# Kernel tuning notes

Measured on AMD Instinct MI355X. Metric: run time of the kernel, lower is better.

The kernel has to match this reference:

```python
import jax, jax.numpy as jnp
import numpy as np

SCALE = 2.0 / 0.24  # UniformBoxWarp(sidelength=0.24)

def pos_embed(x, max_logscale, n_freqs):
    freqs = 2.0 ** jnp.linspace(0.0, float(max_logscale), n_freqs).astype(x.dtype)
    xb = x[..., None, :] * freqs[:, None]                  # (b, n, F, 3)
    sc = jnp.stack([jnp.sin(xb), jnp.cos(xb)], axis=-2)    # (b, n, F, 2, 3)
    sc = sc.reshape(x.shape[:-1] + (n_freqs * 2 * 3,))
    return jnp.concatenate([x, sc], axis=-1)

def film(x, W, b, freq, phase):
    # x: (b, n, in); freq/phase: (b, out) broadcast over points
    h = jnp.einsum('bni,oi->bno', x, W) + b
    return jnp.sin(freq[:, None, :] * h + phase[:, None, :])

def split_style(style):
    # rearrange 'b (2 d) -> b d 2'; freq = first half * 15 + 30, phase = second half
    d = style.shape[-1] // 2
    return style[:, :d] * 15.0 + 30.0, style[:, d:]

def setup_inputs() -> dict:
    key = jax.random.key(0)
    ks = jax.random.split(key, 14)
    B, N, H = 4, 65536, 256
    dim_pos, dim_dir = 63, 27
    r = lambda k, shp, s=1.0: jax.random.normal(k, shp, dtype=jnp.float32) * s
    return {
        'input': r(ks[0], (B, N, 3)),
        'ray_directions': r(ks[1], (B, N, 3)),
        'style_network': r(ks[2], (B, 4 * H)),
        'style_color': r(ks[3], (B, 2 * H)),
        'W1': r(ks[4], (H, dim_pos), 1.0 / dim_pos),
        'b1': jnp.zeros((H,), jnp.float32),
        'W2': r(ks[5], (H, H), np.sqrt(6.0 / H) / 25.0),
        'b2': jnp.zeros((H,), jnp.float32),
        'Wf': r(ks[6], (1, H), np.sqrt(6.0 / H) / 25.0),
        'bf': jnp.zeros((1,), jnp.float32),
        'Wcs': r(ks[7], (H, H + dim_dir), np.sqrt(6.0 / (H + dim_dir)) / 25.0),
        'bcs': jnp.zeros((H,), jnp.float32),
        'Wcl': r(ks[8], (3, H), np.sqrt(6.0 / H) / 25.0),
        'bcl': jnp.zeros((3,), jnp.float32),
    }

def reference(input, ray_directions, style_network, style_color,
              W1, b1, W2, b2, Wf, bf, Wcs, bcs, Wcl, bcl):
    H = W1.shape[0]
    pe = pos_embed(input * SCALE, 9, 10)                 # (b, n, 63)
    fn, pn = split_style(style_network)                  # (b, 2H) each
    x = film(pe, W1, b1, fn[:, :H], pn[:, :H])
    x = film(x, W2, b2, fn[:, H:], pn[:, H:])
    sigma = jnp.einsum('bnh,oh->bno', x, Wf) + bf        # (b, n, 1)
    de = pos_embed(ray_directions, 3, 4)                 # (b, n, 27)
    fc, pc = split_style(style_color)
    hc = film(jnp.concatenate([de, x], axis=-1), Wcs, bcs, fc, pc)
    rgb = jnp.einsum('bnh,oh->bno', hc, Wcl) + bcl       # (b, n, 3)
    return jnp.concatenate([rgb, sigma], axis=-1)        # (b, n, 4)
```

## Files before the change

### kernel.cpp

```cpp
#include <hip/hip_runtime.h>


#define SCALE_F 8.333333333333334f

typedef __attribute__((ext_vector_type(8)))  short sh8;
typedef __attribute__((ext_vector_type(16))) float f32x16;

__device__ __forceinline__ float redrev(float x) {
  const float chi = 0.15915494309189535f;
  const float clo = 6.4206383e-09f;
  float n = rintf(x * chi);
  float d = __builtin_fmaf(x, chi, -n);
  return __builtin_fmaf(x, clo, d);
}
__device__ __forceinline__ float fsin(float x) { return __builtin_amdgcn_sinf(redrev(x)); }
__device__ __forceinline__ float fcos(float x) { return __builtin_amdgcn_cosf(redrev(x)); }

__device__ __forceinline__ unsigned short bfh(float v) {
  unsigned u = __float_as_uint(v);
  return (unsigned short)((u + 0x7fffu + ((u >> 16) & 1u)) >> 16);
}
__device__ __forceinline__ float bf2f(unsigned short h) {
  return __uint_as_float(((unsigned)h) << 16);
}

__global__ void prep_w(const float* __restrict__ W1, const float* __restrict__ W2,
                       const float* __restrict__ Wcs, unsigned short* __restrict__ wsu)
{
  int t = blockIdx.x * 256 + threadIdx.x;
  if (t >= 155648) return;
  int L, pos, base;
  if (t < 16384)      { L = 0; pos = t;         base = 0; }
  else if (t < 81920) { L = 1; pos = t - 16384; base = 32768; }
  else                { L = 2; pos = t - 81920; base = 163840; }
  int kstep = pos >> 12, r = pos & 4095;
  int ot = (r >> 9) & 7, kh = (r >> 8) & 1, o5 = (r >> 3) & 31, j = r & 7;
  int o = ot * 32 + o5, k = kstep * 16 + kh * 8 + j;
  float wv = 0.f;
  if (L == 0)      { if (k < 63) wv = W1[o * 63 + k]; }
  else if (L == 1) { wv = W2[o * 256 + k]; }
  else             { if (k < 27) wv = Wcs[o * 283 + k];
                     else if (k >= 32) wv = Wcs[o * 283 + k - 5]; }
  unsigned short h = bfh(wv);
  unsigned short lo = bfh(wv - bf2f(h));
  wsu[base + kstep * 8192 + r] = h;
  wsu[base + kstep * 8192 + 4096 + r] = lo;
}

template <int NREG>
__device__ __forceinline__ void mfma_layer(
    const unsigned short* __restrict__ prep, int nk,
    const uint4* rBh, const uint4* rBl,
    unsigned short* lW, const unsigned short* lX,
    int myp, int lh, int l31, int ow, int tid, f32x16* acc)
{
  {
    const float4* s = (const float4*)prep;
    ((float4*)lW)[tid] = s[tid];
    ((float4*)lW)[tid + 512] = s[tid + 512];
  }
  __syncthreads();
  #pragma unroll 1
  for (int ks = 0; ks < nk; ++ks) {
    float4 pf0, pf1;
    const bool pre = (ks + 1) < nk;
    if (pre) {
      const float4* s = (const float4*)(prep + (size_t)(ks + 1) * 8192);
      pf0 = s[tid]; pf1 = s[tid + 512];
    }
    sh8 Bh, Bl;
    if (NREG > 0 && ks < NREG) {
      uint4 h = {0,0,0,0}, l = {0,0,0,0};
      #pragma unroll
      for (int rr = 0; rr < NREG; ++rr) if (ks == rr) { h = rBh[rr]; l = rBl[rr]; }
      Bh = __builtin_bit_cast(sh8, h); Bl = __builtin_bit_cast(sh8, l);
    } else {
      const int c0 = (((ks - NREG) * 16 + lh * 8) ^ ((myp & 15) << 3));
      Bh = *(const sh8*)&lX[myp * 256 + c0];
      Bl = *(const sh8*)&lX[32768 + myp * 256 + c0];
    }
    #pragma unroll
    for (int o = 0; o < 4; ++o) {
      const int wb = (ow * 4 + o) * 512 + lh * 256 + l31 * 8;
      sh8 Ah = *(const sh8*)&lW[wb];
      sh8 Al = *(const sh8*)&lW[4096 + wb];
      acc[o] = __builtin_amdgcn_mfma_f32_32x32x16_bf16(Ah, Bh, acc[o], 0, 0, 0);
      acc[o] = __builtin_amdgcn_mfma_f32_32x32x16_bf16(Al, Bh, acc[o], 0, 0, 0);
      acc[o] = __builtin_amdgcn_mfma_f32_32x32x16_bf16(Ah, Bl, acc[o], 0, 0, 0);
    }
    __syncthreads();
    if (pre) { ((float4*)lW)[tid] = pf0; ((float4*)lW)[tid + 512] = pf1; }
    __syncthreads();
  }
}

__device__ __forceinline__ float4 film_g(float4 fr, float4 ph, float a0, float a1, float a2, float a3) {
  float4 r;
  r.x = fsin(__builtin_fmaf(__builtin_fmaf(fr.x, 15.f, 30.f), a0, ph.x));
  r.y = fsin(__builtin_fmaf(__builtin_fmaf(fr.y, 15.f, 30.f), a1, ph.y));
  r.z = fsin(__builtin_fmaf(__builtin_fmaf(fr.z, 15.f, 30.f), a2, ph.z));
  r.w = fsin(__builtin_fmaf(__builtin_fmaf(fr.w, 15.f, 30.f), a3, ph.w));
  return r;
}
__device__ __forceinline__ void store_g(unsigned short* lX, int idx, float4 v) {
  unsigned short h0 = bfh(v.x), h1 = bfh(v.y), h2 = bfh(v.z), h3 = bfh(v.w);
  *(uint2*)&lX[idx] = make_uint2((unsigned)h0 | ((unsigned)h1 << 16),
                                 (unsigned)h2 | ((unsigned)h3 << 16));
  unsigned short l0 = bfh(v.x - bf2f(h0)), l1 = bfh(v.y - bf2f(h1));
  unsigned short l2 = bfh(v.z - bf2f(h2)), l3 = bfh(v.w - bf2f(h3));
  *(uint2*)&lX[32768 + idx] = make_uint2((unsigned)l0 | ((unsigned)l1 << 16),
                                         (unsigned)l2 | ((unsigned)l3 << 16));
}

__global__ void __launch_bounds__(512, 2)
siren_mfma(const float* __restrict__ input, const float* __restrict__ rdir,
           const float* __restrict__ sn, const float* __restrict__ sc,
           const float* __restrict__ b1, const float* __restrict__ b2,
           const float* __restrict__ Wf, const float* __restrict__ bfp,
           const float* __restrict__ bcs, const float* __restrict__ Wcl,
           const float* __restrict__ bcl, const unsigned short* __restrict__ wsu,
           float* __restrict__ out)
{
  __shared__ __align__(16) unsigned short lW[8192];
  __shared__ __align__(16) unsigned short lX[65536];
  __shared__ float lP[8][32][4];

  const int tid = threadIdx.x;
  const int w = tid >> 6, l = tid & 63;
  const int pw = w >> 1, ow = w & 1;
  const int l31 = l & 31, lh = l >> 5;
  const int gpt0 = blockIdx.x * 128;
  const int b = gpt0 >> 16;
  const int myp = pw * 32 + l31;
  const int gp = gpt0 + myp;
  const float* snb = sn + b * 1024;
  const float* scb = sc + b * 512;
  const int swz = (myp & 15) << 3;

  uint4 peh[4], pel[4], deh[2], del[2];
  {
    const float* ip = input + (size_t)gp * 3;
    float x0 = ip[0] * SCALE_F, x1 = ip[1] * SCALE_F, x2 = ip[2] * SCALE_F;
    const float* rp = rdir + (size_t)gp * 3;
    float r0 = rp[0], r1 = rp[1], r2 = rp[2];
    #pragma unroll
    for (int ks = 0; ks < 4; ++ks) {
      unsigned short hh[8], ll[8];
      #pragma unroll
      for (int j = 0; j < 8; ++j) {
        int k = ks * 16 + lh * 8 + j;
        float val;
        if (k >= 63) val = 0.f;
        else if (k < 3) val = (k == 0) ? x0 : (k == 1 ? x1 : x2);
        else {
          int rr = k - 3, f = rr / 6, rem = rr - f * 6;
          int d = (rem < 3) ? rem : rem - 3;
          float xa = (d == 0) ? x0 : (d == 1 ? x1 : x2);
          float arg = xa * (float)(1 << f);
          val = (rem < 3) ? fsin(arg) : fcos(arg);
        }
        hh[j] = bfh(val); ll[j] = bfh(val - bf2f(hh[j]));
      }
      peh[ks] = make_uint4((unsigned)hh[0] | ((unsigned)hh[1] << 16), (unsigned)hh[2] | ((unsigned)hh[3] << 16),
                           (unsigned)hh[4] | ((unsigned)hh[5] << 16), (unsigned)hh[6] | ((unsigned)hh[7] << 16));
      pel[ks] = make_uint4((unsigned)ll[0] | ((unsigned)ll[1] << 16), (unsigned)ll[2] | ((unsigned)ll[3] << 16),
                           (unsigned)ll[4] | ((unsigned)ll[5] << 16), (unsigned)ll[6] | ((unsigned)ll[7] << 16));
    }
    #pragma unroll
    for (int ks = 0; ks < 2; ++ks) {
      unsigned short hh[8], ll[8];
      #pragma unroll
      for (int j = 0; j < 8; ++j) {
        int k = ks * 16 + lh * 8 + j;
        float val;
        if (k >= 27) val = 0.f;
        else if (k < 3) val = (k == 0) ? r0 : (k == 1 ? r1 : r2);
        else {
          int rr = k - 3, f = rr / 6, rem = rr - f * 6;
          int d = (rem < 3) ? rem : rem - 3;
          float ra = (d == 0) ? r0 : (d == 1 ? r1 : r2);
          float arg = ra * (float)(1 << f);
          val = (rem < 3) ? fsin(arg) : fcos(arg);
        }
        hh[j] = bfh(val); ll[j] = bfh(val - bf2f(hh[j]));
      }
      deh[ks] = make_uint4((unsigned)hh[0] | ((unsigned)hh[1] << 16), (unsigned)hh[2] | ((unsigned)hh[3] << 16),
                           (unsigned)hh[4] | ((unsigned)hh[5] << 16), (unsigned)hh[6] | ((unsigned)hh[7] << 16));
      del[ks] = make_uint4((unsigned)ll[0] | ((unsigned)ll[1] << 16), (unsigned)ll[2] | ((unsigned)ll[3] << 16),
                           (unsigned)ll[4] | ((unsigned)ll[5] << 16), (unsigned)ll[6] | ((unsigned)ll[7] << 16));
    }
  }

  f32x16 acc[4];

  #pragma unroll
  for (int o = 0; o < 4; ++o) {
    #pragma unroll
    for (int g = 0; g < 4; ++g) {
      int ob = (ow * 4 + o) * 32 + g * 8 + lh * 4;
      float4 bv = *(const float4*)&b1[ob];
      acc[o][g * 4 + 0] = bv.x; acc[o][g * 4 + 1] = bv.y;
      acc[o][g * 4 + 2] = bv.z; acc[o][g * 4 + 3] = bv.w;
    }
  }
  mfma_layer<4>(wsu + 0, 4, peh, pel, lW, lX, myp, lh, l31, ow, tid, acc);
  #pragma unroll
  for (int o = 0; o < 4; ++o) {
    #pragma unroll
    for (int g = 0; g < 4; ++g) {
      int ob = (ow * 4 + o) * 32 + g * 8 + lh * 4;
      float4 fr = *(const float4*)&snb[ob];
      float4 ph = *(const float4*)&snb[512 + ob];
      float4 vv = film_g(fr, ph, acc[o][g*4+0], acc[o][g*4+1], acc[o][g*4+2], acc[o][g*4+3]);
      store_g(lX, myp * 256 + (ob ^ swz), vv);
    }
  }

  #pragma unroll
  for (int o = 0; o < 4; ++o) {
    #pragma unroll
    for (int g = 0; g < 4; ++g) {
      int ob = (ow * 4 + o) * 32 + g * 8 + lh * 4;
      float4 bv = *(const float4*)&b2[ob];
      acc[o][g * 4 + 0] = bv.x; acc[o][g * 4 + 1] = bv.y;
      acc[o][g * 4 + 2] = bv.z; acc[o][g * 4 + 3] = bv.w;
    }
  }
  mfma_layer<0>(wsu + 32768, 16, nullptr, nullptr, lW, lX, myp, lh, l31, ow, tid, acc);
  float sp = 0.f;
  #pragma unroll
  for (int o = 0; o < 4; ++o) {
    #pragma unroll
    for (int g = 0; g < 4; ++g) {
      int ob = (ow * 4 + o) * 32 + g * 8 + lh * 4;
      float4 fr = *(const float4*)&snb[256 + ob];
      float4 ph = *(const float4*)&snb[768 + ob];
      float4 vv = film_g(fr, ph, acc[o][g*4+0], acc[o][g*4+1], acc[o][g*4+2], acc[o][g*4+3]);
      float4 wf = *(const float4*)&Wf[ob];
      sp = __builtin_fmaf(wf.x, vv.x, sp); sp = __builtin_fmaf(wf.y, vv.y, sp);
      sp = __builtin_fmaf(wf.z, vv.z, sp); sp = __builtin_fmaf(wf.w, vv.w, sp);
      store_g(lX, myp * 256 + (ob ^ swz), vv);
    }
  }
  sp += __shfl_xor(sp, 32);
  lP[w][l31][3] = sp;

  #pragma unroll
  for (int o = 0; o < 4; ++o) {
    #pragma unroll
    for (int g = 0; g < 4; ++g) {
      int ob = (ow * 4 + o) * 32 + g * 8 + lh * 4;
      float4 bv = *(const float4*)&bcs[ob];
      acc[o][g * 4 + 0] = bv.x; acc[o][g * 4 + 1] = bv.y;
      acc[o][g * 4 + 2] = bv.z; acc[o][g * 4 + 3] = bv.w;
    }
  }
  mfma_layer<2>(wsu + 163840, 18, deh, del, lW, lX, myp, lh, l31, ow, tid, acc);
  float q0 = 0.f, q1 = 0.f, q2 = 0.f;
  #pragma unroll
  for (int o = 0; o < 4; ++o) {
    #pragma unroll
    for (int g = 0; g < 4; ++g) {
      int ob = (ow * 4 + o) * 32 + g * 8 + lh * 4;
      float4 fr = *(const float4*)&scb[ob];
      float4 ph = *(const float4*)&scb[256 + ob];
      float4 vv = film_g(fr, ph, acc[o][g*4+0], acc[o][g*4+1], acc[o][g*4+2], acc[o][g*4+3]);
      float4 w0 = *(const float4*)&Wcl[ob];
      float4 w1 = *(const float4*)&Wcl[256 + ob];
      float4 w2 = *(const float4*)&Wcl[512 + ob];
      q0 = __builtin_fmaf(w0.x, vv.x, q0); q0 = __builtin_fmaf(w0.y, vv.y, q0);
      q0 = __builtin_fmaf(w0.z, vv.z, q0); q0 = __builtin_fmaf(w0.w, vv.w, q0);
      q1 = __builtin_fmaf(w1.x, vv.x, q1); q1 = __builtin_fmaf(w1.y, vv.y, q1);
      q1 = __builtin_fmaf(w1.z, vv.z, q1); q1 = __builtin_fmaf(w1.w, vv.w, q1);
      q2 = __builtin_fmaf(w2.x, vv.x, q2); q2 = __builtin_fmaf(w2.y, vv.y, q2);
      q2 = __builtin_fmaf(w2.z, vv.z, q2); q2 = __builtin_fmaf(w2.w, vv.w, q2);
    }
  }
  q0 += __shfl_xor(q0, 32); q1 += __shfl_xor(q1, 32); q2 += __shfl_xor(q2, 32);
  lP[w][l31][0] = q0; lP[w][l31][1] = q1; lP[w][l31][2] = q2;
  __syncthreads();

  {
    int pt = tid >> 2, ch = tid & 3, pv = pt >> 5;
    float v = lP[pv * 2][pt & 31][ch] + lP[pv * 2 + 1][pt & 31][ch];
    v += (ch == 3) ? bfp[0] : bcl[ch];
    out[(size_t)gpt0 * 4 + tid] = v;
  }
}

extern "C" void kernel_launch(void* const* d_in, const int* in_sizes, int n_in,
                              void* d_out, int out_size, void* d_ws, size_t ws_size,
                              hipStream_t stream) {
  const float* input = (const float*)d_in[0];
  const float* rdir  = (const float*)d_in[1];
  const float* sn    = (const float*)d_in[2];
  const float* sc    = (const float*)d_in[3];
  const float* W1    = (const float*)d_in[4];
  const float* b1    = (const float*)d_in[5];
  const float* W2    = (const float*)d_in[6];
  const float* b2    = (const float*)d_in[7];
  const float* Wf    = (const float*)d_in[8];
  const float* bf    = (const float*)d_in[9];
  const float* Wcs   = (const float*)d_in[10];
  const float* bcs   = (const float*)d_in[11];
  const float* Wcl   = (const float*)d_in[12];
  const float* bcl   = (const float*)d_in[13];
  unsigned short* wsu = (unsigned short*)d_ws;
  float* out = (float*)d_out;

  prep_w<<<608, 256, 0, stream>>>(W1, W2, Wcs, wsu);
  siren_mfma<<<2048, 512, 0, stream>>>(input, rdir, sn, sc, b1, b2, Wf, bf,
                                       bcs, Wcl, bcl, wsu, out);
}
```

Measured before the change: 333.7 us.

## Switch split-precision MFMA to fp16 with scaled residuals and 2x2 wave tiling

Replaces the bf16 hi/lo split with an fp16 hi plus a 1024-scaled fp16 residual for both weights and activations. Each wave now computes 2 output tiles × 2 point tiles instead of 4 output tiles × 1 point tile, which changes per-wave data reuse. The positional embedding is now staged cooperatively through LDS, and the sine argument reduction is folded into the FiLM constants. Shared memory grows to about 144KB, dropping occupancy to one block per CU. The fp16 residual scaling also risks reduced range or underflow precision.

```diff
diff --git a/kernel.cpp b/kernel.cpp
--- a/kernel.cpp
+++ b/kernel.cpp
@@ -3,7 +3,8 @@
 
 #define SCALE_F 8.333333333333334f
 
-typedef __attribute__((ext_vector_type(8)))  short sh8;
+typedef _Float16 hf;
+typedef __attribute__((ext_vector_type(8)))  _Float16 hf8;
 typedef __attribute__((ext_vector_type(16))) float f32x16;
 
 __device__ __forceinline__ float redrev(float x) {
@@ -15,13 +16,18 @@
 }
 __device__ __forceinline__ float fsin(float x) { return __builtin_amdgcn_sinf(redrev(x)); }
 __device__ __forceinline__ float fcos(float x) { return __builtin_amdgcn_cosf(redrev(x)); }
-
-__device__ __forceinline__ unsigned short bfh(float v) {
-  unsigned u = __float_as_uint(v);
-  return (unsigned short)((u + 0x7fffu + ((u >> 16) & 1u)) >> 16);
-}
-__device__ __forceinline__ float bf2f(unsigned short h) {
-  return __uint_as_float(((unsigned)h) << 16);
+__device__ __forceinline__ float sinrev(float t) { return __builtin_amdgcn_sinf(t - rintf(t)); }
+
+#define INV2PI 0.15915494309189535f
+#define C15R   2.3873241463784303f
+#define C30R   4.7746482927568605f
+
+__device__ __forceinline__ unsigned pk2h(hf a, hf b) {
+  return ((unsigned)__builtin_bit_cast(unsigned short, a)) |
+         (((unsigned)__builtin_bit_cast(unsigned short, b)) << 16);
+}
+__device__ __forceinline__ int swadr(int pt, int slot) {
+  return pt * 256 + ((slot ^ (pt & 7)) << 3);
 }
 
 __global__ void prep_w(const float* __restrict__ W1, const float* __restrict__ W2,
@@ -39,54 +45,79 @@
   float wv = 0.f;
   if (L == 0)      { if (k < 63) wv = W1[o * 63 + k]; }
   else if (L == 1) { wv = W2[o * 256 + k]; }
-  else             { if (k < 27) wv = Wcs[o * 283 + k];
-                     else if (k >= 32) wv = Wcs[o * 283 + k - 5]; }
-  unsigned short h = bfh(wv);
-  unsigned short lo = bfh(wv - bf2f(h));
-  wsu[base + kstep * 8192 + r] = h;
-  wsu[base + kstep * 8192 + 4096 + r] = lo;
-}
-
-template <int NREG>
-__device__ __forceinline__ void mfma_layer(
-    const unsigned short* __restrict__ prep, int nk,
-    const uint4* rBh, const uint4* rBl,
-    unsigned short* lW, const unsigned short* lX,
-    int myp, int lh, int l31, int ow, int tid, f32x16* acc)
+  else { if (k < 256) wv = Wcs[o * 283 + 27 + k];
+         else { int q = k - 256; if (q < 27) wv = Wcs[o * 283 + q]; } }
+  hf hh = (hf)wv;
+  hf ll = (hf)((wv - (float)hh) * 1024.0f);
+  wsu[base + kstep * 8192 + r]        = __builtin_bit_cast(unsigned short, hh);
+  wsu[base + kstep * 8192 + 4096 + r] = __builtin_bit_cast(unsigned short, ll);
+}
+
+__device__ __forceinline__ float peval(float x0, float x1, float x2, int k) {
+  if (k >= 63) return 0.f;
+  if (k < 3) return (k == 0) ? x0 : ((k == 1) ? x1 : x2);
+  int rr = k - 3, f = rr / 6, rem = rr - f * 6;
+  int d = (rem < 3) ? rem : rem - 3;
+  float xa = (d == 0) ? x0 : ((d == 1) ? x1 : x2);
+  float arg = xa * (float)(1 << f);
+  return (rem < 3) ? fsin(arg) : fcos(arg);
+}
+__device__ __forceinline__ float deval(float r0, float r1, float r2, int k) {
+  if (k >= 27) return 0.f;
+  if (k < 3) return (k == 0) ? r0 : ((k == 1) ? r1 : r2);
+  int rr = k - 3, f = rr / 6, rem = rr - f * 6;
+  int d = (rem < 3) ? rem : rem - 3;
+  float ra = (d == 0) ? r0 : ((d == 1) ? r1 : r2);
+  float arg = ra * (float)(1 << f);
+  return (rem < 3) ? fsin(arg) : fcos(arg);
+}
+
+template <int NK, bool DE>
+__device__ __forceinline__ void layer_loop(
+    const unsigned short* __restrict__ prep,
+    unsigned short* __restrict__ lW, const unsigned short* __restrict__ lX,
+    f32x16 acc[2][2], int tid, int ow, int ptA, int ptB, int h, int l31,
+    const hf8* deBh, const hf8* deBl)
 {
   {
-    const float4* s = (const float4*)prep;
-    ((float4*)lW)[tid] = s[tid];
-    ((float4*)lW)[tid + 512] = s[tid + 512];
+    const float4* s0 = (const float4*)prep;
+    ((float4*)lW)[tid] = s0[tid];
+    ((float4*)lW)[tid + 512] = s0[tid + 512];
   }
   __syncthreads();
   #pragma unroll 1
-  for (int ks = 0; ks < nk; ++ks) {
+  for (int ks = 0; ks < NK; ++ks) {
     float4 pf0, pf1;
-    const bool pre = (ks + 1) < nk;
+    const bool pre = (ks + 1) < NK;
     if (pre) {
       const float4* s = (const float4*)(prep + (size_t)(ks + 1) * 8192);
       pf0 = s[tid]; pf1 = s[tid + 512];
     }
-    sh8 Bh, Bl;
-    if (NREG > 0 && ks < NREG) {
-      uint4 h = {0,0,0,0}, l = {0,0,0,0};
-      #pragma unroll
-      for (int rr = 0; rr < NREG; ++rr) if (ks == rr) { h = rBh[rr]; l = rBl[rr]; }
-      Bh = __builtin_bit_cast(sh8, h); Bl = __builtin_bit_cast(sh8, l);
+    hf8 Bh0, Bh1, Bl0, Bl1;
+    if (!DE || ks < NK - 2) {
+      Bh0 = *(const hf8*)&lX[swadr(ptA, ks * 2 + h)];
+      Bh1 = *(const hf8*)&lX[swadr(ptB, ks * 2 + h)];
+      Bl0 = *(const hf8*)&lX[32768 + swadr(ptA, ks * 2 + h)];
+      Bl1 = *(const hf8*)&lX[32768 + swadr(ptB, ks * 2 + h)];
     } else {
-      const int c0 = (((ks - NREG) * 16 + lh * 8) ^ ((myp & 15) << 3));
-      Bh = *(const sh8*)&lX[myp * 256 + c0];
-      Bl = *(const sh8*)&lX[32768 + myp * 256 + c0];
-    }
-    #pragma unroll
-    for (int o = 0; o < 4; ++o) {
-      const int wb = (ow * 4 + o) * 512 + lh * 256 + l31 * 8;
-      sh8 Ah = *(const sh8*)&lW[wb];
-      sh8 Al = *(const sh8*)&lW[4096 + wb];
-      acc[o] = __builtin_amdgcn_mfma_f32_32x32x16_bf16(Ah, Bh, acc[o], 0, 0, 0);
-      acc[o] = __builtin_amdgcn_mfma_f32_32x32x16_bf16(Al, Bh, acc[o], 0, 0, 0);
-      acc[o] = __builtin_amdgcn_mfma_f32_32x32x16_bf16(Ah, Bl, acc[o], 0, 0, 0);
+      int ksl = ks - (NK - 2);
+      Bh0 = deBh[ksl * 2 + 0]; Bh1 = deBh[ksl * 2 + 1];
+      Bl0 = deBl[ksl * 2 + 0]; Bl1 = deBl[ksl * 2 + 1];
+    }
+    const hf sc = (hf)0.0009765625f;
+    hf8 Bh0s = Bh0 * sc, Bh1s = Bh1 * sc;
+    hf8 Bl0s = Bl0 * sc, Bl1s = Bl1 * sc;
+    #pragma unroll
+    for (int oi = 0; oi < 2; ++oi) {
+      const int wb = (ow * 2 + oi) * 512 + h * 256 + l31 * 8;
+      hf8 Ah = *(const hf8*)&lW[wb];
+      hf8 Al = *(const hf8*)&lW[4096 + wb];
+      acc[oi][0] = __builtin_amdgcn_mfma_f32_32x32x16_f16(Ah, Bh0,  acc[oi][0], 0, 0, 0);
+      acc[oi][0] = __builtin_amdgcn_mfma_f32_32x32x16_f16(Al, Bh0s, acc[oi][0], 0, 0, 0);
+      acc[oi][0] = __builtin_amdgcn_mfma_f32_32x32x16_f16(Ah, Bl0s, acc[oi][0], 0, 0, 0);
+      acc[oi][1] = __builtin_amdgcn_mfma_f32_32x32x16_f16(Ah, Bh1,  acc[oi][1], 0, 0, 0);
+      acc[oi][1] = __builtin_amdgcn_mfma_f32_32x32x16_f16(Al, Bh1s, acc[oi][1], 0, 0, 0);
+      acc[oi][1] = __builtin_amdgcn_mfma_f32_32x32x16_f16(Ah, Bl1s, acc[oi][1], 0, 0, 0);
     }
     __syncthreads();
     if (pre) { ((float4*)lW)[tid] = pf0; ((float4*)lW)[tid + 512] = pf1; }
@@ -94,25 +125,18 @@
   }
 }
 
-__device__ __forceinline__ float4 film_g(float4 fr, float4 ph, float a0, float a1, float a2, float a3) {
-  float4 r;
-  r.x = fsin(__builtin_fmaf(__builtin_fmaf(fr.x, 15.f, 30.f), a0, ph.x));
-  r.y = fsin(__builtin_fmaf(__builtin_fmaf(fr.y, 15.f, 30.f), a1, ph.y));
-  r.z = fsin(__builtin_fmaf(__builtin_fmaf(fr.z, 15.f, 30.f), a2, ph.z));
-  r.w = fsin(__builtin_fmaf(__builtin_fmaf(fr.w, 15.f, 30.f), a3, ph.w));
-  return r;
-}
-__device__ __forceinline__ void store_g(unsigned short* lX, int idx, float4 v) {
-  unsigned short h0 = bfh(v.x), h1 = bfh(v.y), h2 = bfh(v.z), h3 = bfh(v.w);
-  *(uint2*)&lX[idx] = make_uint2((unsigned)h0 | ((unsigned)h1 << 16),
-                                 (unsigned)h2 | ((unsigned)h3 << 16));
-  unsigned short l0 = bfh(v.x - bf2f(h0)), l1 = bfh(v.y - bf2f(h1));
-  unsigned short l2 = bfh(v.z - bf2f(h2)), l3 = bfh(v.w - bf2f(h3));
-  *(uint2*)&lX[32768 + idx] = make_uint2((unsigned)l0 | ((unsigned)l1 << 16),
-                                         (unsigned)l2 | ((unsigned)l3 << 16));
-}
-
-__global__ void __launch_bounds__(512, 2)
+__device__ __forceinline__ void store_pair(unsigned short* lX, int pt, int slot, int off,
+                                           float v0, float v1, float v2, float v3)
+{
+  hf h0 = (hf)v0, h1 = (hf)v1, h2 = (hf)v2, h3 = (hf)v3;
+  int base = pt * 256 + ((slot ^ (pt & 7)) << 3) + off;
+  *(uint2*)&lX[base] = make_uint2(pk2h(h0, h1), pk2h(h2, h3));
+  hf r0 = (hf)((v0 - (float)h0) * 1024.f), r1 = (hf)((v1 - (float)h1) * 1024.f);
+  hf r2 = (hf)((v2 - (float)h2) * 1024.f), r3 = (hf)((v3 - (float)h3) * 1024.f);
+  *(uint2*)&lX[32768 + base] = make_uint2(pk2h(r0, r1), pk2h(r2, r3));
+}
+
+__global__ void __launch_bounds__(512, 1)
 siren_mfma(const float* __restrict__ input, const float* __restrict__ rdir,
            const float* __restrict__ sn, const float* __restrict__ sc,
            const float* __restrict__ b1, const float* __restrict__ b2,
@@ -121,170 +145,194 @@
            const float* __restrict__ bcl, const unsigned short* __restrict__ wsu,
            float* __restrict__ out)
 {
-  __shared__ __align__(16) unsigned short lW[8192];
-  __shared__ __align__(16) unsigned short lX[65536];
-  __shared__ float lP[8][32][4];
+  __shared__ __align__(16) unsigned char smem[147456];
+  unsigned short* lX = (unsigned short*)smem;
+  unsigned short* lW = (unsigned short*)(smem + 131072);
+  float* lP = (float*)smem;
 
   const int tid = threadIdx.x;
   const int w = tid >> 6, l = tid & 63;
-  const int pw = w >> 1, ow = w & 1;
-  const int l31 = l & 31, lh = l >> 5;
-  const int gpt0 = blockIdx.x * 128;
-  const int b = gpt0 >> 16;
-  const int myp = pw * 32 + l31;
-  const int gp = gpt0 + myp;
+  const int ow = w >> 1, pw = w & 1;
+  const int l31 = l & 31, h = l >> 5;
+  const int gpt0 = blockIdx.x << 7;
+  const int b = blockIdx.x >> 9;
+  const int ptA = pw * 64 + l31, ptB = ptA + 32;
   const float* snb = sn + b * 1024;
   const float* scb = sc + b * 512;
-  const int swz = (myp & 15) << 3;
-
-  uint4 peh[4], pel[4], deh[2], del[2];
+
+  float rA0, rA1, rA2, rB0, rB1, rB2;
   {
-    const float* ip = input + (size_t)gp * 3;
+    const float* rp = rdir + (size_t)(gpt0 + ptA) * 3;
+    rA0 = rp[0]; rA1 = rp[1]; rA2 = rp[2];
+    const float* rq = rdir + (size_t)(gpt0 + ptB) * 3;
+    rB0 = rq[0]; rB1 = rq[1]; rB2 = rq[2];
+  }
+
+  {
+    const int ept = tid & 127, eseg = tid >> 7;
+    const float* ip = input + (size_t)(gpt0 + ept) * 3;
     float x0 = ip[0] * SCALE_F, x1 = ip[1] * SCALE_F, x2 = ip[2] * SCALE_F;
-    const float* rp = rdir + (size_t)gp * 3;
-    float r0 = rp[0], r1 = rp[1], r2 = rp[2];
-    #pragma unroll
-    for (int ks = 0; ks < 4; ++ks) {
-      unsigned short hh[8], ll[8];
+    #pragma unroll
+    for (int j = 0; j < 4; ++j) {
+      int k0 = eseg * 16 + 4 * j;
+      float v0 = peval(x0, x1, x2, k0),     v1 = peval(x0, x1, x2, k0 + 1);
+      float v2 = peval(x0, x1, x2, k0 + 2), v3 = peval(x0, x1, x2, k0 + 3);
+      int slot = eseg * 2 + (j >> 1);
+      store_pair(lX, ept, slot, (j & 1) * 4, v0, v1, v2, v3);
+    }
+  }
+  __syncthreads();
+
+  f32x16 acc[2][2];
+  float sp0 = 0.f, sp1 = 0.f;
+
+  #pragma unroll
+  for (int oi = 0; oi < 2; ++oi)
+    #pragma unroll
+    for (int q = 0; q < 4; ++q) {
+      int o0 = ow * 64 + oi * 32 + q * 8 + h * 4;
+      float4 bv = *(const float4*)&b1[o0];
+      acc[oi][0][q*4+0] = bv.x; acc[oi][0][q*4+1] = bv.y; acc[oi][0][q*4+2] = bv.z; acc[oi][0][q*4+3] = bv.w;
+      acc[oi][1][q*4+0] = bv.x; acc[oi][1][q*4+1] = bv.y; acc[oi][1][q*4+2] = bv.z; acc[oi][1][q*4+3] = bv.w;
+    }
+  layer_loop<4, false>(wsu, lW, lX, acc, tid, ow, ptA, ptB, h, l31, nullptr, nullptr);
+  #pragma unroll
+  for (int oi = 0; oi < 2; ++oi)
+    #pragma unroll
+    for (int q = 0; q < 4; ++q) {
+      int o0 = ow * 64 + oi * 32 + q * 8 + h * 4;
+      float4 f4 = *(const float4*)&snb[o0];
+      float4 p4 = *(const float4*)&snb[512 + o0];
+      float fr0 = __builtin_fmaf(f4.x, C15R, C30R), fr1 = __builtin_fmaf(f4.y, C15R, C30R);
+      float fr2 = __builtin_fmaf(f4.z, C15R, C30R), fr3 = __builtin_fmaf(f4.w, C15R, C30R);
+      float pr0 = p4.x * INV2PI, pr1 = p4.y * INV2PI, pr2 = p4.z * INV2PI, pr3 = p4.w * INV2PI;
+      int slot = ow * 8 + oi * 4 + q;
       #pragma unroll
-      for (int j = 0; j < 8; ++j) {
-        int k = ks * 16 + lh * 8 + j;
-        float val;
-        if (k >= 63) val = 0.f;
-        else if (k < 3) val = (k == 0) ? x0 : (k == 1 ? x1 : x2);
-        else {
-          int rr = k - 3, f = rr / 6, rem = rr - f * 6;
-          int d = (rem < 3) ? rem : rem - 3;
-          float xa = (d == 0) ? x0 : (d == 1 ? x1 : x2);
-          float arg = xa * (float)(1 << f);
-          val = (rem < 3) ? fsin(arg) : fcos(arg);
-        }
-        hh[j] = bfh(val); ll[j] = bfh(val - bf2f(hh[j]));
+      for (int pi = 0; pi < 2; ++pi) {
+        float v0 = sinrev(__builtin_fmaf(fr0, acc[oi][pi][q*4+0], pr0));
+        float v1 = sinrev(__builtin_fmaf(fr1, acc[oi][pi][q*4+1], pr1));
+        float v2 = sinrev(__builtin_fmaf(fr2, acc[oi][pi][q*4+2], pr2));
+        float v3 = sinrev(__builtin_fmaf(fr3, acc[oi][pi][q*4+3], pr3));
+        int pt = (pi == 0) ? ptA : ptB;
+        store_pair(lX, pt, slot, h * 4, v0, v1, v2, v3);
       }
-      peh[ks] = make_uint4((unsigned)hh[0] | ((unsigned)hh[1] << 16), (unsigned)hh[2] | ((unsigned)hh[3] << 16),
-                           (unsigned)hh[4] | ((unsigned)hh[5] << 16), (unsigned)hh[6] | ((unsigned)hh[7] << 16));
-      pel[ks] = make_uint4((unsigned)ll[0] | ((unsigned)ll[1] << 16), (unsigned)ll[2] | ((unsigned)ll[3] << 16),
-                           (unsigned)ll[4] | ((unsigned)ll[5] << 16), (unsigned)ll[6] | ((unsigned)ll[7] << 16));
-    }
-    #pragma unroll
-    for (int ks = 0; ks < 2; ++ks) {
-      unsigned short hh[8], ll[8];
+    }
+
+  #pragma unroll
+  for (int oi = 0; oi < 2; ++oi)
+    #pragma unroll
+    for (int q = 0; q < 4; ++q) {
+      int o0 = ow * 64 + oi * 32 + q * 8 + h * 4;
+      float4 bv = *(const float4*)&b2[o0];
+      acc[oi][0][q*4+0] = bv.x; acc[oi][0][q*4+1] = bv.y; acc[oi][0][q*4+2] = bv.z; acc[oi][0][q*4+3] = bv.w;
+      acc[oi][1][q*4+0] = bv.x; acc[oi][1][q*4+1] = bv.y; acc[oi][1][q*4+2] = bv.z; acc[oi][1][q*4+3] = bv.w;
+    }
+  layer_loop<16, false>(wsu + 32768, lW, lX, acc, tid, ow, ptA, ptB, h, l31, nullptr, nullptr);
+  #pragma unroll
+  for (int oi = 0; oi < 2; ++oi)
+    #pragma unroll
+    for (int q = 0; q < 4; ++q) {
+      int o0 = ow * 64 + oi * 32 + q * 8 + h * 4;
+      float4 f4 = *(const float4*)&snb[256 + o0];
+      float4 p4 = *(const float4*)&snb[768 + o0];
+      float4 wf = *(const float4*)&Wf[o0];
+      float fr0 = __builtin_fmaf(f4.x, C15R, C30R), fr1 = __builtin_fmaf(f4.y, C15R, C30R);
+      float fr2 = __builtin_fmaf(f4.z, C15R, C30R), fr3 = __builtin_fmaf(f4.w, C15R, C30R);
+      float pr0 = p4.x * INV2PI, pr1 = p4.y * INV2PI, pr2 = p4.z * INV2PI, pr3 = p4.w * INV2PI;
+      int slot = ow * 8 + oi * 4 + q;
       #pragma unroll
-      for (int j = 0; j < 8; ++j) {
-        int k = ks * 16 + lh * 8 + j;
-        float val;
-        if (k >= 27) val = 0.f;
-        else if (k < 3) val = (k == 0) ? r0 : (k == 1 ? r1 : r2);
-        else {
-          int rr = k - 3, f = rr / 6, rem = rr - f * 6;
-          int d = (rem < 3) ? rem : rem - 3;
-          float ra = (d == 0) ? r0 : (d == 1 ? r1 : r2);
-          float arg = ra * (float)(1 << f);
-          val = (rem < 3) ? fsin(arg) : fcos(arg);
-        }
-        hh[j] = bfh(val); ll[j] = bfh(val - bf2f(hh[j]));
+      for (int pi = 0; pi < 2; ++pi) {
+        float v0 = sinrev(__builtin_fmaf(fr0, acc[oi][pi][q*4+0], pr0));
+        float v1 = sinrev(__builtin_fmaf(fr1, acc[oi][pi][q*4+1], pr1));
+        float v2 = sinrev(__builtin_fmaf(fr2, acc[oi][pi][q*4+2], pr2));
+        float v3 = sinrev(__builtin_fmaf(fr3, acc[oi][pi][q*4+3], pr3));
+        float s = __builtin_fmaf(wf.x, v0, __builtin_fmaf(wf.y, v1,
+                  __builtin_fmaf(wf.z, v2, wf.w * v3)));
+        if (pi == 0) sp0 += s; else sp1 += s;
+        int pt = (pi == 0) ? ptA : ptB;
+        store_pair(lX, pt, slot, h * 4, v0, v1, v2, v3);
       }
-      deh[ks] = make_uint4((unsigned)hh[0] | ((unsigned)hh[1] << 16), (unsigned)hh[2] | ((unsigned)hh[3] << 16),
-                           (unsigned)hh[4] | ((unsigned)hh[5] << 16), (unsigned)hh[6] | ((unsigned)hh[7] << 16));
-      del[ks] = make_uint4((unsigned)ll[0] | ((unsigned)ll[1] << 16), (unsigned)ll[2] | ((unsigned)ll[3] << 16),
-                           (unsigned)ll[4] | ((unsigned)ll[5] << 16), (unsigned)ll[6] | ((unsigned)ll[7] << 16));
-    }
-  }
-
-  f32x16 acc[4];
-
-  #pragma unroll
-  for (int o = 0; o < 4; ++o) {
-    #pragma unroll
-    for (int g = 0; g < 4; ++g) {
-      int ob = (ow * 4 + o) * 32 + g * 8 + lh * 4;
-      float4 bv = *(const float4*)&b1[ob];
-      acc[o][g * 4 + 0] = bv.x; acc[o][g * 4 + 1] = bv.y;
-      acc[o][g * 4 + 2] = bv.z; acc[o][g * 4 + 3] = bv.w;
-    }
-  }
-  mfma_layer<4>(wsu + 0, 4, peh, pel, lW, lX, myp, lh, l31, ow, tid, acc);
-  #pragma unroll
-  for (int o = 0; o < 4; ++o) {
-    #pragma unroll
-    for (int g = 0; g < 4; ++g) {
-      int ob = (ow * 4 + o) * 32 + g * 8 + lh * 4;
-      float4 fr = *(const float4*)&snb[ob];
-      float4 ph = *(const float4*)&snb[512 + ob];
-      float4 vv = film_g(fr, ph, acc[o][g*4+0], acc[o][g*4+1], acc[o][g*4+2], acc[o][g*4+3]);
-      store_g(lX, myp * 256 + (ob ^ swz), vv);
-    }
-  }
-
-  #pragma unroll
-  for (int o = 0; o < 4; ++o) {
-    #pragma unroll
-    for (int g = 0; g < 4; ++g) {
-      int ob = (ow * 4 + o) * 32 + g * 8 + lh * 4;
-      float4 bv = *(const float4*)&b2[ob];
-      acc[o][g * 4 + 0] = bv.x; acc[o][g * 4 + 1] = bv.y;
-      acc[o][g * 4 + 2] = bv.z; acc[o][g * 4 + 3] = bv.w;
-    }
-  }
-  mfma_layer<0>(wsu + 32768, 16, nullptr, nullptr, lW, lX, myp, lh, l31, ow, tid, acc);
-  float sp = 0.f;
-  #pragma unroll
-  for (int o = 0; o < 4; ++o) {
-    #pragma unroll
-    for (int g = 0; g < 4; ++g) {
-      int ob = (ow * 4 + o) * 32 + g * 8 + lh * 4;
-      float4 fr = *(const float4*)&snb[256 + ob];
-      float4 ph = *(const float4*)&snb[768 + ob];
-      float4 vv = film_g(fr, ph, acc[o][g*4+0], acc[o][g*4+1], acc[o][g*4+2], acc[o][g*4+3]);
-      float4 wf = *(const float4*)&Wf[ob];
-      sp = __builtin_fmaf(wf.x, vv.x, sp); sp = __builtin_fmaf(wf.y, vv.y, sp);
-      sp = __builtin_fmaf(wf.z, vv.z, sp); sp = __builtin_fmaf(wf.w, vv.w, sp);
-      store_g(lX, myp * 256 + (ob ^ swz), vv);
-    }
-  }
-  sp += __shfl_xor(sp, 32);
-  lP[w][l31][3] = sp;
-
-  #pragma unroll
-  for (int o = 0; o < 4; ++o) {
-    #pragma unroll
-    for (int g = 0; g < 4; ++g) {
-      int ob = (ow * 4 + o) * 32 + g * 8 + lh * 4;
-      float4 bv = *(const float4*)&bcs[ob];
-      acc[o][g * 4 + 0] = bv.x; acc[o][g * 4 + 1] = bv.y;
-      acc[o][g * 4 + 2] = bv.z; acc[o][g * 4 + 3] = bv.w;
-    }
-  }
-  mfma_layer<2>(wsu + 163840, 18, deh, del, lW, lX, myp, lh, l31, ow, tid, acc);
-  float q0 = 0.f, q1 = 0.f, q2 = 0.f;
-  #pragma unroll
-  for (int o = 0; o < 4; ++o) {
-    #pragma unroll
-    for (int g = 0; g < 4; ++g) {
-      int ob = (ow * 4 + o) * 32 + g * 8 + lh * 4;
-      float4 fr = *(const float4*)&scb[ob];
-      float4 ph = *(const float4*)&scb[256 + ob];
-      float4 vv = film_g(fr, ph, acc[o][g*4+0], acc[o][g*4+1], acc[o][g*4+2], acc[o][g*4+3]);
-      float4 w0 = *(const float4*)&Wcl[ob];
-      float4 w1 = *(const float4*)&Wcl[256 + ob];
-      float4 w2 = *(const float4*)&Wcl[512 + ob];
-      q0 = __builtin_fmaf(w0.x, vv.x, q0); q0 = __builtin_fmaf(w0.y, vv.y, q0);
-      q0 = __builtin_fmaf(w0.z, vv.z, q0); q0 = __builtin_fmaf(w0.w, vv.w, q0);
-      q1 = __builtin_fmaf(w1.x, vv.x, q1); q1 = __builtin_fmaf(w1.y, vv.y, q1);
-      q1 = __builtin_fmaf(w1.z, vv.z, q1); q1 = __builtin_fmaf(w1.w, vv.w, q1);
-      q2 = __builtin_fmaf(w2.x, vv.x, q2); q2 = __builtin_fmaf(w2.y, vv.y, q2);
-      q2 = __builtin_fmaf(w2.z, vv.z, q2); q2 = __builtin_fmaf(w2.w, vv.w, q2);
-    }
-  }
-  q0 += __shfl_xor(q0, 32); q1 += __shfl_xor(q1, 32); q2 += __shfl_xor(q2, 32);
-  lP[w][l31][0] = q0; lP[w][l31][1] = q1; lP[w][l31][2] = q2;
+    }
+
+  hf8 deBh[4], deBl[4];
+  #pragma unroll
+  for (int ksl = 0; ksl < 2; ++ksl)
+    #pragma unroll
+    for (int pi = 0; pi < 2; ++pi) {
+      float r0 = (pi == 0) ? rA0 : rB0, r1 = (pi == 0) ? rA1 : rB1, r2 = (pi == 0) ? rA2 : rB2;
+      unsigned uh[4], ul[4];
+      #pragma unroll
+      for (int jj = 0; jj < 4; ++jj) {
+        int k = ksl * 16 + h * 8 + 2 * jj;
+        float va = deval(r0, r1, r2, k), vb = deval(r0, r1, r2, k + 1);
+        hf ha = (hf)va, hb = (hf)vb;
+        uh[jj] = pk2h(ha, hb);
+        ul[jj] = pk2h((hf)((va - (float)ha) * 1024.f), (hf)((vb - (float)hb) * 1024.f));
+      }
+      uint4 vh = make_uint4(uh[0], uh[1], uh[2], uh[3]);
+      uint4 vl = make_uint4(ul[0], ul[1], ul[2], ul[3]);
+      deBh[ksl * 2 + pi] = __builtin_bit_cast(hf8, vh);
+      deBl[ksl * 2 + pi] = __builtin_bit_cast(hf8, vl);
+    }
+
+  #pragma unroll
+  for (int oi = 0; oi < 2; ++oi)
+    #pragma unroll
+    for (int q = 0; q < 4; ++q) {
+      int o0 = ow * 64 + oi * 32 + q * 8 + h * 4;
+      float4 bv = *(const float4*)&bcs[o0];
+      acc[oi][0][q*4+0] = bv.x; acc[oi][0][q*4+1] = bv.y; acc[oi][0][q*4+2] = bv.z; acc[oi][0][q*4+3] = bv.w;
+      acc[oi][1][q*4+0] = bv.x; acc[oi][1][q*4+1] = bv.y; acc[oi][1][q*4+2] = bv.z; acc[oi][1][q*4+3] = bv.w;
+    }
+  layer_loop<18, true>(wsu + 163840, lW, lX, acc, tid, ow, ptA, ptB, h, l31, deBh, deBl);
+  float q00 = 0.f, q01 = 0.f, q02 = 0.f, q10 = 0.f, q11 = 0.f, q12 = 0.f;
+  #pragma unroll
+  for (int oi = 0; oi < 2; ++oi)
+    #pragma unroll
+    for (int q = 0; q < 4; ++q) {
+      int o0 = ow * 64 + oi * 32 + q * 8 + h * 4;
+      float4 f4 = *(const float4*)&scb[o0];
+      float4 p4 = *(const float4*)&scb[256 + o0];
+      float4 w0 = *(const float4*)&Wcl[o0];
+      float4 w1 = *(const float4*)&Wcl[256 + o0];
+      float4 w2 = *(const float4*)&Wcl[512 + o0];
+      float fr0 = __builtin_fmaf(f4.x, C15R, C30R), fr1 = __builtin_fmaf(f4.y, C15R, C30R);
+      float fr2 = __builtin_fmaf(f4.z, C15R, C30R), fr3 = __builtin_fmaf(f4.w, C15R, C30R);
+      float pr0 = p4.x * INV2PI, pr1 = p4.y * INV2PI, pr2 = p4.z * INV2PI, pr3 = p4.w * INV2PI;
+      #pragma unroll
+      for (int pi = 0; pi < 2; ++pi) {
+        float v0 = sinrev(__builtin_fmaf(fr0, acc[oi][pi][q*4+0], pr0));
+        float v1 = sinrev(__builtin_fmaf(fr1, acc[oi][pi][q*4+1], pr1));
+        float v2 = sinrev(__builtin_fmaf(fr2, acc[oi][pi][q*4+2], pr2));
+        float v3 = sinrev(__builtin_fmaf(fr3, acc[oi][pi][q*4+3], pr3));
+        float a0 = __builtin_fmaf(w0.x, v0, __builtin_fmaf(w0.y, v1, __builtin_fmaf(w0.z, v2, w0.w * v3)));
+        float a1 = __builtin_fmaf(w1.x, v0, __builtin_fmaf(w1.y, v1, __builtin_fmaf(w1.z, v2, w1.w * v3)));
+        float a2 = __builtin_fmaf(w2.x, v0, __builtin_fmaf(w2.y, v1, __builtin_fmaf(w2.z, v2, w2.w * v3)));
+        if (pi == 0) { q00 += a0; q01 += a1; q02 += a2; }
+        else         { q10 += a0; q11 += a1; q12 += a2; }
+      }
+    }
+
+  q00 += __shfl_xor(q00, 32); q01 += __shfl_xor(q01, 32); q02 += __shfl_xor(q02, 32);
+  q10 += __shfl_xor(q10, 32); q11 += __shfl_xor(q11, 32); q12 += __shfl_xor(q12, 32);
+  sp0 += __shfl_xor(sp0, 32); sp1 += __shfl_xor(sp1, 32);
+  if (h == 0) {
+    *(float4*)&lP[((w * 2 + 0) * 32 + l31) * 4] = make_float4(q00, q01, q02, sp0);
+    *(float4*)&lP[((w * 2 + 1) * 32 + l31) * 4] = make_float4(q10, q11, q12, sp1);
+  }
   __syncthreads();
 
   {
-    int pt = tid >> 2, ch = tid & 3, pv = pt >> 5;
-    float v = lP[pv * 2][pt & 31][ch] + lP[pv * 2 + 1][pt & 31][ch];
+    int ptL = tid >> 2, ch = tid & 3;
+    int pwt = ptL >> 6, pit = (ptL >> 5) & 1, lt = ptL & 31;
+    float v = 0.f;
+    #pragma unroll
+    for (int owt = 0; owt < 4; ++owt) {
+      int wv_ = (owt * 2 + pwt);
+      v += lP[((wv_ * 2 + pit) * 32 + lt) * 4 + ch];
+    }
     v += (ch == 3) ? bfp[0] : bcl[ch];
-    out[(size_t)gpt0 * 4 + tid] = v;
+    out[((size_t)gpt0 + ptL) * 4 + ch] = v;
   }
 }
 
```

New measurement: 407.0 us. +22.0%, slower.
